# Performance work log

Measured on AMD Instinct MI355X. Metric: run time of the kernel, lower is better.

The kernel has to match this reference:

```python
import jax, jax.numpy as jnp
import numpy as np


def _gelu(v):
    return jax.nn.gelu(v, approximate=False)


def _conv1x1(x, W, b):
    # x: [B, Ci, H, W], W: [Co, Ci]
    return jnp.einsum('bixy,oi->boxy', x, W) + b[None, :, None, None]


def _spectral(x, w1r, w2r, m1, m2):
    # x: [B, Ci, H, W]; w*r: [Ci, Co, m1, m2, 2] (real/imag)
    w1 = w1r[..., 0] + 1j * w1r[..., 1]
    w2 = w2r[..., 0] + 1j * w2r[..., 1]
    B, C, H, W = x.shape
    xf = jnp.fft.rfft2(x)  # [B, Ci, H, W//2+1] complex64
    o1 = jnp.einsum('bixy,ioxy->boxy', xf[:, :, :m1, :m2], w1)
    o2 = jnp.einsum('bixy,ioxy->boxy', xf[:, :, H - m1:, :m2], w2)
    Co = w1.shape[1]
    of = jnp.zeros((B, Co, H, W // 2 + 1), dtype=xf.dtype)
    of = of.at[:, :, :m1, :m2].set(o1)
    of = of.at[:, :, H - m1:, :m2].set(o2)
    return jnp.fft.irfft2(of, s=(H, W))


def _pool(x):
    B, C, H, W = x.shape
    return x.reshape(B, C, H // 2, 2, W // 2, 2).mean(axis=(3, 5))


def _up(x):
    # matches torch F.interpolate(scale_factor=2, mode='bilinear', align_corners=False)
    B, C, H, W = x.shape
    return jax.image.resize(x, (B, C, 2 * H, 2 * W), method='bilinear')


def _forward(x, fcin_w, fcin_b, sc1_w1, sc1_w2, c1_w, c1_b, sc2_w1, sc2_w2, c2_w, c2_b,
             scb_w1, scb_w2, cb_w, cb_b, su2_w1, su2_w2, u2_w, u2_b,
             su1_w1, su1_w2, u1_w, u1_b, fc1_w, fc1_b, fc2_w, fc2_b):
    v = jnp.einsum('bhwi,oi->bhwo', x, fcin_w) + fcin_b   # lift 6 -> width
    v = v.transpose(0, 3, 1, 2)                            # [B, C, H, W]
    x1 = _gelu(_spectral(v, sc1_w1, sc1_w2, 12, 12) + _conv1x1(v, c1_w, c1_b))
    x1d = _pool(x1)
    x2 = _gelu(_spectral(x1d, sc2_w1, sc2_w2, 8, 8) + _conv1x1(x1d, c2_w, c2_b))
    x2d = _pool(x2)
    xb = _gelu(_spectral(x2d, scb_w1, scb_w2, 4, 4) + _conv1x1(x2d, cb_w, cb_b))
    x2c = jnp.concatenate([_up(xb), x2], axis=1)           # [B, 3.5w, H/2, W/2]
    x2o = _gelu(_spectral(x2c, su2_w1, su2_w2, 8, 8) + _conv1x1(x2c, u2_w, u2_b))
    x1c = jnp.concatenate([_up(x2o), x1], axis=1)          # [B, 2.5w, H, W]
    x1o = _gelu(_spectral(x1c, su1_w1, su1_w2, 12, 12) + _conv1x1(x1c, u1_w, u1_b))
    h = x1o.transpose(0, 2, 3, 1)
    h = _gelu(jnp.einsum('bhwi,oi->bhwo', h, fc1_w) + fc1_b)
    return jnp.einsum('bhwi,oi->bhwo', h, fc2_w) + fc2_b   # [B, H, W, 3]


def setup_inputs() -> dict:
    key = jax.random.key(0)
    ks = jax.random.split(key, 20)

    def cw(k, ci, co, m):  # complex spectral weight stored as [...,2] real
        return (1.0 / (ci * co)) * jax.random.normal(k, (ci, co, m, m, 2), dtype=jnp.float32)

    def lin(k, o, i):
        k1, k2 = jax.random.split(k)
        lim = 1.0 / np.sqrt(i)
        return (jax.random.uniform(k1, (o, i), jnp.float32, -lim, lim),
                jax.random.uniform(k2, (o,), jnp.float32, -lim, lim))

    d = {}
    d['x'] = jax.random.normal(ks[0], (4, 256, 256, 6), dtype=jnp.float32)
    d['fcin_w'], d['fcin_b'] = lin(ks[1], 64, 6)
    d['sc1_w1'] = cw(ks[2], 64, 64, 12); d['sc1_w2'] = cw(ks[3], 64, 64, 12)
    d['c1_w'], d['c1_b'] = lin(ks[4], 64, 64)
    d['sc2_w1'] = cw(ks[5], 64, 96, 8); d['sc2_w2'] = cw(ks[6], 64, 96, 8)
    d['c2_w'], d['c2_b'] = lin(ks[7], 96, 64)
    d['scb_w1'] = cw(ks[8], 96, 128, 4); d['scb_w2'] = cw(ks[9], 96, 128, 4)
    d['cb_w'], d['cb_b'] = lin(ks[10], 128, 96)
    d['su2_w1'] = cw(ks[11], 224, 96, 8); d['su2_w2'] = cw(ks[12], 224, 96, 8)
    d['u2_w'], d['u2_b'] = lin(ks[13], 96, 224)
    d['su1_w1'] = cw(ks[14], 160, 64, 12); d['su1_w2'] = cw(ks[15], 160, 64, 12)
    d['u1_w'], d['u1_b'] = lin(ks[16], 64, 160)
    d['fc1_w'], d['fc1_b'] = lin(ks[17], 256, 64)
    d['fc2_w'], d['fc2_b'] = lin(ks[18], 3, 256)
    return d


def reference(x, fcin_w, fcin_b, sc1_w1, sc1_w2, c1_w, c1_b, sc2_w1, sc2_w2, c2_w, c2_b,
              scb_w1, scb_w2, cb_w, cb_b, su2_w1, su2_w2, u2_w, u2_b,
              su1_w1, su1_w2, u1_w, u1_b, fc1_w, fc1_b, fc2_w, fc2_b):
    return _forward(x, fcin_w, fcin_b, sc1_w1, sc1_w2, c1_w, c1_b, sc2_w1, sc2_w2, c2_w, c2_b,
                    scb_w1, scb_w2, cb_w, cb_b, su2_w1, su2_w2, u2_w, u2_b,
                    su1_w1, su1_w2, u1_w, u1_b, fc1_w, fc1_b, fc2_w, fc2_b)
```

## Files before the change

### kernel.cpp

```cpp
#include <hip/hip_runtime.h>
#include <math.h>
#include <cstdio>


__device__ __forceinline__ float gelu_f(float v) {
    return 0.5f * v * (1.0f + erff(v * 0.70710678118654752f));
}

__global__ __launch_bounds__(256) void init_tw_kernel(float2* tw) {
    int t = threadIdx.x;
    tw[t] = make_float2(cospif(t * (1.0f / 128.0f)), sinpif(t * (1.0f / 128.0f)));
}

__global__ __launch_bounds__(256) void transpose_mat_kernel(const float* __restrict__ src,
                                                            float* __restrict__ dst,
                                                            int Co, int Ci) {
    int idx = blockIdx.x * blockDim.x + threadIdx.x;
    if (idx >= Ci * Co) return;
    int o = idx % Co; int i = idx / Co;
    dst[idx] = src[(size_t)o * Ci + i];
}

template <int M2, int SRC, int W_T>
__global__ __launch_bounds__(256, 4) void dftx_kernel(
    const float* __restrict__ U, int C, int Coff, int Ctot,
    int H, int Hs, int Ws,
    const float* __restrict__ liftW, const float* __restrict__ liftB,
    int stepW, const float2* __restrict__ tw, float2* __restrict__ Fx) {
    constexpr int W = W_T;
    constexpr int WS2 = W_T / 2;
    __shared__ float2 twxk[(SRC == 2) ? (WS2 * M2) : (W * M2)];
    int tid = threadIdx.x;
    if constexpr (SRC == 2) {
        for (int t = tid; t < WS2 * M2; t += 256) {
            int j = t / M2, k = t - (t / M2) * M2;
            float wr = 0.f, wi = 0.f;
            auto addE = [&](int xx, float w) {
                float2 e = tw[(xx * k * stepW) & 255];
                wr += w * e.x; wi += w * e.y;
            };
            if (j == 0)            { addE(0, 1.0f); addE(1, 0.75f); addE(2, 0.25f); }
            else if (j == WS2 - 1) { addE(2 * j - 1, 0.25f); addE(2 * j, 0.75f); addE(2 * j + 1, 1.0f); }
            else                   { addE(2 * j - 1, 0.25f); addE(2 * j, 0.75f);
                                     addE(2 * j + 1, 0.75f); addE(2 * j + 2, 0.25f); }
            twxk[t] = make_float2(wr, wi);
        }
    } else {
        for (int t = tid; t < W * M2; t += 256) {
            int x = t / M2, k = t - (t / M2) * M2;
            twxk[t] = tw[(x * k * stepW) & 255];
        }
    }
    __syncthreads();
    int by = blockIdx.x * 4 + (tid >> 6);
    int c = blockIdx.y * 64 + (tid & 63);
    if (c >= C) return;

    const float* rowD = nullptr;
    const float* Sa = nullptr; const float* Sb = nullptr;
    float wy = 0.f, bc = 0.f;
    float w6[6] = {0, 0, 0, 0, 0, 0};
    if constexpr (SRC == 0) {
        rowD = U + (size_t)by * W * C + c;
    } else if constexpr (SRC == 1) {
        bc = liftB[c];
#pragma unroll
        for (int j = 0; j < 6; j++) w6[j] = liftW[c * 6 + j];
    } else {
        int b = by / H, y = by % H;
        float fy = 0.5f * y - 0.25f;
        int y0 = (int)floorf(fy); wy = fy - y0;
        int ya = y0 < 0 ? 0 : y0;
        int yb = (y0 + 1 > Hs - 1) ? Hs - 1 : y0 + 1;
        Sa = U + ((size_t)(b * Hs + ya) * Ws) * C + c;
        Sb = U + ((size_t)(b * Hs + yb) * Ws) * C + c;
    }

    float ar[M2], ai[M2];
#pragma unroll
    for (int k = 0; k < M2; k++) { ar[k] = 0.f; ai[k] = 0.f; }
    if constexpr (SRC == 2) {
        for (int js = 0; js < WS2; js++) {
            float sa = Sa[(size_t)js * C], sb = Sb[(size_t)js * C];
            float u = sa * (1.f - wy) + sb * wy;
            const float4* gp = (const float4*)&twxk[js * M2];
#pragma unroll
            for (int k2 = 0; k2 < M2 / 2; k2++) {
                float4 g4 = gp[k2];
                ar[2 * k2] += u * g4.x;     ai[2 * k2] -= u * g4.y;
                ar[2 * k2 + 1] += u * g4.z; ai[2 * k2 + 1] -= u * g4.w;
            }
        }
    } else {
        for (int x = 0; x < W; x++) {
            float u;
            if constexpr (SRC == 0) {
                u = rowD[(size_t)x * C];
            } else {
                const float* xp = U + ((size_t)by * W + x) * 6;
                u = bc;
#pragma unroll
                for (int j = 0; j < 6; j++) u += w6[j] * xp[j];
            }
            const float4* wp = (const float4*)&twxk[x * M2];
#pragma unroll
            for (int k2 = 0; k2 < M2 / 2; k2++) {
                float4 t4 = wp[k2];
                ar[2 * k2] += u * t4.x;     ai[2 * k2] -= u * t4.y;
                ar[2 * k2 + 1] += u * t4.z; ai[2 * k2 + 1] -= u * t4.w;
            }
        }
    }
    float2* o = Fx + ((size_t)by * M2) * Ctot + Coff + c;
#pragma unroll
    for (int k = 0; k < M2; k++) o[(size_t)k * Ctot] = make_float2(ar[k], ai[k]);
}

template <int M1>
__global__ __launch_bounds__(256, 2) void dfty2_kernel(
    const float2* __restrict__ Fx, int H, int m2, int Ct,
    int stepH, const float2* __restrict__ tw, float2* __restrict__ XF) {
    constexpr int NKY = 2 * M1;
    __shared__ float twc[256], tws[256];
    __shared__ float2 red[3][NKY][64];
    int tid = threadIdx.x;
    for (int t = tid; t < 256; t += 256) {
        float2 v = tw[t]; twc[t] = v.x; tws[t] = v.y;
    }
    __syncthreads();
    int kx = blockIdx.x % m2; int ct = blockIdx.x / m2;
    int b = blockIdx.y;
    int lane = tid & 63, grp = tid >> 6;
    int c = ct * 64 + lane;
    float ar[NKY], ai[NKY];
#pragma unroll
    for (int k = 0; k < NKY; k++) { ar[k] = 0.f; ai[k] = 0.f; }
    if (c < Ct) {
        int ylen = H >> 2;
        int y0 = grp * ylen;
        const float2* base = Fx + ((size_t)(b * H + y0) * m2 + kx) * Ct + c;
        size_t stride = (size_t)m2 * Ct;
        for (int yy = 0; yy < ylen; yy++) {
            float2 f = base[(size_t)yy * stride];
            int a = ((y0 + yy) * stepH) & 255;
            int t = 0;
#pragma unroll
            for (int j = 0; j < M1; j++) {
                float cc = twc[t], ss = tws[t];
                ar[j] += f.x * cc + f.y * ss;
                ai[j] += f.y * cc - f.x * ss;
                t = (t + a) & 255;
            }
            t = (M1 * 256 - M1 * a) & 255;
#pragma unroll
            for (int j = 0; j < M1; j++) {
                float cc = twc[t], ss = tws[t];
                ar[M1 + j] += f.x * cc + f.y * ss;
                ai[M1 + j] += f.y * cc - f.x * ss;
                t = (t + a) & 255;
            }
        }
    }
    if (grp > 0) {
#pragma unroll
        for (int k = 0; k < NKY; k++) red[grp - 1][k][lane] = make_float2(ar[k], ai[k]);
    }
    __syncthreads();
    if (grp == 0 && c < Ct) {
#pragma unroll
        for (int k = 0; k < NKY; k++) {
            float2 r0 = red[0][k][lane], r1 = red[1][k][lane], r2 = red[2][k][lane];
            XF[((size_t)(b * NKY + k) * m2 + kx) * Ct + c] =
                make_float2(ar[k] + r0.x + r1.x + r2.x, ai[k] + r0.y + r1.y + r2.y);
        }
    }
}

__global__ __launch_bounds__(128, 2) void modemix2_kernel(
    const float2* __restrict__ XF,
    const float* __restrict__ w1f, const float* __restrict__ w2f,
    int Ci, int Co, int m1, int m2, float2* __restrict__ OF) {
    __shared__ float2 xsm[4][224];
    int mode = blockIdx.x;
    int nmode = 2 * m1 * m2;
    for (int t = threadIdx.x; t < 4 * Ci; t += blockDim.x) {
        int b = t / Ci, i = t - b * Ci;
        xsm[b][i] = XF[((size_t)b * nmode + mode) * Ci + i];
    }
    __syncthreads();
    int o = threadIdx.x;
    if (o >= Co) return;
    int kx = mode % m2; int kyi = mode / m2;
    const float2* w = (const float2*)((kyi < m1) ? w1f : w2f);
    int ky = (kyi < m1) ? kyi : (kyi - m1);
    float ar0 = 0, ai0 = 0, ar1 = 0, ai1 = 0, ar2 = 0, ai2 = 0, ar3 = 0, ai3 = 0;
    for (int i = 0; i < Ci; i++) {
        float2 wv = w[(((size_t)i * Co + o) * m1 + ky) * m2 + kx];
        float2 a = xsm[0][i], b2 = xsm[1][i], c2 = xsm[2][i], d2 = xsm[3][i];
        ar0 += a.x * wv.x - a.y * wv.y;  ai0 += a.x * wv.y + a.y * wv.x;
        ar1 += b2.x * wv.x - b2.y * wv.y; ai1 += b2.x * wv.y + b2.y * wv.x;
        ar2 += c2.x * wv.x - c2.y * wv.y; ai2 += c2.x * wv.y + c2.y * wv.x;
        ar3 += d2.x * wv.x - d2.y * wv.y; ai3 += d2.x * wv.y + d2.y * wv.x;
    }
    OF[((size_t)0 * nmode + mode) * Co + o] = make_float2(ar0, ai0);
    OF[((size_t)1 * nmode + mode) * Co + o] = make_float2(ar1, ai1);
    OF[((size_t)2 * nmode + mode) * Co + o] = make_float2(ar2, ai2);
    OF[((size_t)3 * nmode + mode) * Co + o] = make_float2(ar3, ai3);
}

__global__ __launch_bounds__(256, 4) void idfty_kernel(
    const float2* __restrict__ OF, int H, int m1, int m2, int Co,
    int stepH, const float2* __restrict__ tw, float2* __restrict__ Gy, int N) {
    __shared__ float twc[256], tws[256];
    for (int t = threadIdx.x; t < 256; t += blockDim.x) {
        float2 v = tw[t]; twc[t] = v.x; tws[t] = v.y;
    }
    __syncthreads();
    int idx = blockIdx.x * blockDim.x + threadIdx.x;
    if (idx >= N) return;
    int o = idx % Co; int r = idx / Co;
    int kx = r % m2;  r /= m2;
    int y = r % H;    int b = r / H;
    float accr = 0.f, acci = 0.f;
    for (int kyi = 0; kyi < 2 * m1; kyi++) {
        int ky = (kyi < m1) ? kyi : (H - 2 * m1 + kyi);
        int t = (ky * y * stepH) & 255;
        float2 f = OF[((size_t)(b * 2 * m1 + kyi) * m2 + kx) * Co + o];
        float cc = twc[t], ss = tws[t];
        accr += f.x * cc - f.y * ss;
        acci += f.x * ss + f.y * cc;
    }
    Gy[idx] = make_float2(accr, acci);
}

template <int SRCA, bool HASB, int CO, int CI, int M2, int PG, int MINW>
__global__ __launch_bounds__((CO / 8) * PG, MINW) void synth_kernel(
    const float2* __restrict__ Gy,
    const float* __restrict__ A, int CA, int HsA, int WsA,
    const float* __restrict__ UB, int CB,
    const float* __restrict__ liftW, const float* __restrict__ liftB,
    const float* __restrict__ WcT, const float* __restrict__ bias,
    int H, int W, int stepW, float invHW,
    const float2* __restrict__ tw, float* __restrict__ out) {
    constexpr int OO = CO / 8;
    constexpr int BLK = OO * PG;
    constexpr int P = PG * 4;
    constexpr int CIP = CI + 1;
    __shared__ float xs[P][CIP];
    __shared__ float2 twL[M2][P];
    int tid = threadIdx.x;
    int pix0 = blockIdx.x * P;
    int x0 = pix0 % W;  int by = pix0 / W;
    for (int t = tid; t < M2 * P; t += BLK) {
        int k = t / P, p = t - (t / P) * P;
        float2 v = tw[((x0 + p) * k * stepW) & 255];
        float s = ((k == 0) ? 1.f : 2.f) * invHW;
        twL[k][p] = make_float2(s * v.x, s * v.y);
    }
    for (int t = tid; t < P * CI; t += BLK) {
        int p = t / CI, i = t - p * CI;
        int pix = pix0 + p;
        float val;
        if (HASB && i >= CA) {
            val = UB[(size_t)pix * CB + (i - CA)];
        } else if constexpr (SRCA == 0) {
            val = A[(size_t)pix * CA + i];
        } else if constexpr (SRCA == 1) {
            const float* xp = A + (size_t)pix * 6;
            float a = liftB[i];
#pragma unroll
            for (int j = 0; j < 6; j++) a += xp[j] * liftW[i * 6 + j];
            val = a;
        } else {
            int xx = pix % W; int r = pix / W; int y = r % H; int b = r / H;
            float fy = 0.5f * y - 0.25f, fx = 0.5f * xx - 0.25f;
            int y0 = (int)floorf(fy); float wy = fy - y0;
            int x0i = (int)floorf(fx); float wx = fx - x0i;
            int ya = y0 < 0 ? 0 : y0;
            int yb = (y0 + 1 > HsA - 1) ? HsA - 1 : y0 + 1;
            int xa = x0i < 0 ? 0 : x0i;
            int xb2 = (x0i + 1 > WsA - 1) ? WsA - 1 : x0i + 1;
            const float* base = A + ((size_t)b * HsA * WsA) * CA + i;
            float v00 = base[((size_t)ya * WsA + xa) * CA];
            float v01 = base[((size_t)ya * WsA + xb2) * CA];
            float v10 = base[((size_t)yb * WsA + xa) * CA];
            float v11 = base[((size_t)yb * WsA + xb2) * CA];
            val = (1.f - wy) * ((1.f - wx) * v00 + wx * v01) +
                  wy * ((1.f - wx) * v10 + wx * v11);
        }
        xs[p][i] = val;
    }
    __syncthreads();
    int oo = tid % OO, pg = tid / OO;
    float acc[4][8];
#pragma unroll
    for (int q = 0; q < 4; q++)
#pragma unroll
        for (int j = 0; j < 8; j++) acc[q][j] = 0.f;
    const float2* grow = Gy + ((size_t)by * M2) * CO + oo * 8;
#pragma unroll
    for (int k = 0; k < M2; k++) {
        float4 g0 = *(const float4*)&grow[(size_t)k * CO + 0];
        float4 g1 = *(const float4*)&grow[(size_t)k * CO + 2];
        float4 g2 = *(const float4*)&grow[(size_t)k * CO + 4];
        float4 g3 = *(const float4*)&grow[(size_t)k * CO + 6];
#pragma unroll
        for (int q = 0; q < 4; q++) {
            float2 tq = twL[k][pg * 4 + q];
            acc[q][0] += g0.x * tq.x - g0.y * tq.y;
            acc[q][1] += g0.z * tq.x - g0.w * tq.y;
            acc[q][2] += g1.x * tq.x - g1.y * tq.y;
            acc[q][3] += g1.z * tq.x - g1.w * tq.y;
            acc[q][4] += g2.x * tq.x - g2.y * tq.y;
            acc[q][5] += g2.z * tq.x - g2.w * tq.y;
            acc[q][6] += g3.x * tq.x - g3.y * tq.y;
            acc[q][7] += g3.z * tq.x - g3.w * tq.y;
        }
    }
    const float* wrow = WcT + oo * 8;
#pragma unroll 4
    for (int i = 0; i < CI; i++) {
        float4 wa = *(const float4*)&wrow[(size_t)i * CO];
        float4 wb = *(const float4*)&wrow[(size_t)i * CO + 4];
#pragma unroll
        for (int q = 0; q < 4; q++) {
            float a = xs[pg * 4 + q][i];
            acc[q][0] += a * wa.x; acc[q][1] += a * wa.y;
            acc[q][2] += a * wa.z; acc[q][3] += a * wa.w;
            acc[q][4] += a * wb.x; acc[q][5] += a * wb.y;
            acc[q][6] += a * wb.z; acc[q][7] += a * wb.w;
        }
    }
    float4 ba = *(const float4*)&bias[oo * 8];
    float4 bb = *(const float4*)&bias[oo * 8 + 4];
#pragma unroll
    for (int q = 0; q < 4; q++) {
        int pix = pix0 + pg * 4 + q;
        float4 r0, r1;
        r0.x = gelu_f(acc[q][0] + ba.x);
        r0.y = gelu_f(acc[q][1] + ba.y);
        r0.z = gelu_f(acc[q][2] + ba.z);
        r0.w = gelu_f(acc[q][3] + ba.w);
        r1.x = gelu_f(acc[q][4] + bb.x);
        r1.y = gelu_f(acc[q][5] + bb.y);
        r1.z = gelu_f(acc[q][6] + bb.z);
        r1.w = gelu_f(acc[q][7] + bb.w);
        *(float4*)&out[(size_t)pix * CO + oo * 8] = r0;
        *(float4*)&out[(size_t)pix * CO + oo * 8 + 4] = r1;
    }
}

__global__ __launch_bounds__(256, 2) void head_kernel(
    const float* __restrict__ xin, const float* __restrict__ fc1t,
    const float* __restrict__ fc1b, const float* __restrict__ fc2w,
    const float* __restrict__ fc2b, float* __restrict__ out) {
    __shared__ float xs[16][65];
    __shared__ float red[64][49];
    int tid = threadIdx.x;
    int pix0 = blockIdx.x * 16;
    const float* src = xin + (size_t)pix0 * 64;
    for (int t = tid; t < 16 * 64; t += 256) xs[t >> 6][t & 63] = src[t];
    __syncthreads();
    int jq = tid & 63, pg = tid >> 6;
    float acc[4][4];
#pragma unroll
    for (int q = 0; q < 4; q++)
#pragma unroll
        for (int j = 0; j < 4; j++) acc[q][j] = 0.f;
    const float* wrow = fc1t + jq * 4;
    for (int i = 0; i < 64; i++) {
        float4 w = *(const float4*)&wrow[(size_t)i * 256];
#pragma unroll
        for (int q = 0; q < 4; q++) {
            float a = xs[pg * 4 + q][i];
            acc[q][0] += a * w.x; acc[q][1] += a * w.y;
            acc[q][2] += a * w.z; acc[q][3] += a * w.w;
        }
    }
    float4 b1 = *(const float4*)&fc1b[jq * 4];
    float4 w20 = *(const float4*)&fc2w[0 * 256 + jq * 4];
    float4 w21 = *(const float4*)&fc2w[1 * 256 + jq * 4];
    float4 w22 = *(const float4*)&fc2w[2 * 256 + jq * 4];
#pragma unroll
    for (int q = 0; q < 4; q++) {
        float h0 = gelu_f(acc[q][0] + b1.x);
        float h1 = gelu_f(acc[q][1] + b1.y);
        float h2 = gelu_f(acc[q][2] + b1.z);
        float h3 = gelu_f(acc[q][3] + b1.w);
        int col = (pg * 4 + q) * 3;
        red[jq][col + 0] = h0 * w20.x + h1 * w20.y + h2 * w20.z + h3 * w20.w;
        red[jq][col + 1] = h0 * w21.x + h1 * w21.y + h2 * w21.z + h3 * w21.w;
        red[jq][col + 2] = h0 * w22.x + h1 * w22.y + h2 * w22.z + h3 * w22.w;
    }
    __syncthreads();
    if (tid < 48) {
        float s = 0.f;
        for (int j = 0; j < 64; j++) s += red[j][tid];
        int px = tid / 3, o3 = tid - 3 * px;
        out[(size_t)(pix0 + px) * 3 + o3] = s + fc2b[o3];
    }
}

__global__ __launch_bounds__(256, 4) void pool_kernel(
    const float* __restrict__ in, float* __restrict__ out,
    int H2, int W2, int C, int N) {
    int idx = blockIdx.x * blockDim.x + threadIdx.x;
    if (idx >= N) return;
    int c = idx % C; int r = idx / C;
    int xo = r % W2; r /= W2;
    int yo = r % H2; int b = r / H2;
    int W = W2 * 2;
    const float* p = in + (((size_t)(b * (H2 * 2) + 2 * yo) * W) + 2 * xo) * C + c;
    float v = p[0] + p[C] + p[(size_t)W * C] + p[(size_t)W * C + C];
    out[idx] = 0.25f * v;
}


static inline unsigned nb_(size_t n, int b) { return (unsigned)((n + b - 1) / b); }

extern "C" void kernel_launch(void* const* d_in, const int* in_sizes, int n_in,
                              void* d_out, int out_size, void* d_ws, size_t ws_size,
                              hipStream_t stream) {
    (void)in_sizes; (void)n_in; (void)out_size;
    const float* x      = (const float*)d_in[0];
    const float* fcin_w = (const float*)d_in[1];
    const float* fcin_b = (const float*)d_in[2];
    const float* sc1_w1 = (const float*)d_in[3];
    const float* sc1_w2 = (const float*)d_in[4];
    const float* c1_w   = (const float*)d_in[5];
    const float* c1_b   = (const float*)d_in[6];
    const float* sc2_w1 = (const float*)d_in[7];
    const float* sc2_w2 = (const float*)d_in[8];
    const float* c2_w   = (const float*)d_in[9];
    const float* c2_b   = (const float*)d_in[10];
    const float* scb_w1 = (const float*)d_in[11];
    const float* scb_w2 = (const float*)d_in[12];
    const float* cb_w   = (const float*)d_in[13];
    const float* cb_b   = (const float*)d_in[14];
    const float* su2_w1 = (const float*)d_in[15];
    const float* su2_w2 = (const float*)d_in[16];
    const float* u2_w   = (const float*)d_in[17];
    const float* u2_b   = (const float*)d_in[18];
    const float* su1_w1 = (const float*)d_in[19];
    const float* su1_w2 = (const float*)d_in[20];
    const float* u1_w   = (const float*)d_in[21];
    const float* u1_b   = (const float*)d_in[22];
    const float* fc1_w  = (const float*)d_in[23];
    const float* fc1_b  = (const float*)d_in[24];
    const float* fc2_w  = (const float*)d_in[25];
    const float* fc2_b  = (const float*)d_in[26];
    float* out = (float*)d_out;

    float* wsf = (float*)d_ws;
    size_t off = 0;
    auto alloc = [&](size_t nfloats) -> float* {
        float* p = wsf + off;
        off += (nfloats + 63) & ~(size_t)63;
        return p;
    };

    float2* tw = (float2*)alloc(512);
    float* c1t  = alloc(64 * 64);
    float* c2t  = alloc(64 * 96);
    float* cbt  = alloc(96 * 128);
    float* u2t  = alloc(224 * 96);
    float* u1t  = alloc(160 * 64);
    float* fc1t = alloc(64 * 256);

    float* x1  = alloc((size_t)4 * 256 * 256 * 64);
    float* x1d = alloc((size_t)4 * 128 * 128 * 64);
    float* x2  = alloc((size_t)4 * 128 * 128 * 96);
    float* xb  = alloc((size_t)4 * 64 * 64 * 128);
    float* x2o = alloc((size_t)4 * 128 * 128 * 96);

    float2* Fx = (float2*)alloc((size_t)2 * 4 * 256 * 12 * 160);
    float2* XF = (float2*)alloc((size_t)2 * 4 * 24 * 12 * 160);
    float2* OF = (float2*)alloc((size_t)2 * 4 * 24 * 12 * 128);
    float2* Gy = (float2*)alloc((size_t)2 * 4 * 256 * 12 * 96);

    size_t need = off * sizeof(float);
    if (ws_size < need) {
        fprintf(stderr, "[FNO2d] workspace too small: need %zu bytes, have %zu\n",
                need, ws_size);
        return;
    }
    float* x2d = x1d;

    init_tw_kernel<<<1, 256, 0, stream>>>(tw);
    transpose_mat_kernel<<<nb_(64 * 64, 256), 256, 0, stream>>>(c1_w, c1t, 64, 64);
    transpose_mat_kernel<<<nb_(64 * 96, 256), 256, 0, stream>>>(c2_w, c2t, 96, 64);
    transpose_mat_kernel<<<nb_(96 * 128, 256), 256, 0, stream>>>(cb_w, cbt, 128, 96);
    transpose_mat_kernel<<<nb_(224 * 96, 256), 256, 0, stream>>>(u2_w, u2t, 96, 224);
    transpose_mat_kernel<<<nb_(160 * 64, 256), 256, 0, stream>>>(u1_w, u1t, 64, 160);
    transpose_mat_kernel<<<nb_(64 * 256, 256), 256, 0, stream>>>(fc1_w, fc1t, 256, 64);

    int N;

    dftx_kernel<12, 1, 256><<<dim3(256, 1), 256, 0, stream>>>(
        x, 64, 0, 64, 256, 0, 0, fcin_w, fcin_b, 1, tw, Fx);
    dfty2_kernel<12><<<dim3(12, 4), 256, 0, stream>>>(Fx, 256, 12, 64, 1, tw, XF);
    modemix2_kernel<<<288, 128, 0, stream>>>(XF, sc1_w1, sc1_w2, 64, 64, 12, 12, OF);
    N = 4 * 256 * 12 * 64;
    idfty_kernel<<<nb_(N, 256), 256, 0, stream>>>(OF, 256, 12, 12, 64, 1, tw, Gy, N);
    synth_kernel<1, false, 64, 64, 12, 16, 3><<<4 * 256 * 256 / 64, 128, 0, stream>>>(
        Gy, x, 64, 0, 0, nullptr, 0, fcin_w, fcin_b, c1t, c1_b,
        256, 256, 1, 1.0f / 65536.0f, tw, x1);
    N = 4 * 128 * 128 * 64;
    pool_kernel<<<nb_(N, 256), 256, 0, stream>>>(x1, x1d, 128, 128, 64, N);

    dftx_kernel<8, 0, 128><<<dim3(128, 1), 256, 0, stream>>>(
        x1d, 64, 0, 64, 128, 0, 0, nullptr, nullptr, 2, tw, Fx);
    dfty2_kernel<8><<<dim3(8, 4), 256, 0, stream>>>(Fx, 128, 8, 64, 2, tw, XF);
    modemix2_kernel<<<128, 128, 0, stream>>>(XF, sc2_w1, sc2_w2, 64, 96, 8, 8, OF);
    N = 4 * 128 * 8 * 96;
    idfty_kernel<<<nb_(N, 256), 256, 0, stream>>>(OF, 128, 8, 8, 96, 2, tw, Gy, N);
    synth_kernel<0, false, 96, 64, 8, 16, 2><<<4 * 128 * 128 / 64, 192, 0, stream>>>(
        Gy, x1d, 64, 0, 0, nullptr, 0, nullptr, nullptr, c2t, c2_b,
        128, 128, 2, 1.0f / 16384.0f, tw, x2);
    N = 4 * 64 * 64 * 96;
    pool_kernel<<<nb_(N, 256), 256, 0, stream>>>(x2, x2d, 64, 64, 96, N);

    dftx_kernel<4, 0, 64><<<dim3(64, 2), 256, 0, stream>>>(
        x2d, 96, 0, 96, 64, 0, 0, nullptr, nullptr, 4, tw, Fx);
    dfty2_kernel<4><<<dim3(4 * 2, 4), 256, 0, stream>>>(Fx, 64, 4, 96, 4, tw, XF);
    modemix2_kernel<<<32, 128, 0, stream>>>(XF, scb_w1, scb_w2, 96, 128, 4, 4, OF);
    N = 4 * 64 * 4 * 128;
    idfty_kernel<<<nb_(N, 256), 256, 0, stream>>>(OF, 64, 4, 4, 128, 4, tw, Gy, N);
    synth_kernel<0, false, 128, 96, 4, 8, 2><<<4 * 64 * 64 / 32, 128, 0, stream>>>(
        Gy, x2d, 96, 0, 0, nullptr, 0, nullptr, nullptr, cbt, cb_b,
        64, 64, 4, 1.0f / 4096.0f, tw, xb);

    dftx_kernel<8, 2, 128><<<dim3(128, 2), 256, 0, stream>>>(
        xb, 128, 0, 224, 128, 64, 64, nullptr, nullptr, 2, tw, Fx);
    dftx_kernel<8, 0, 128><<<dim3(128, 2), 256, 0, stream>>>(
        x2, 96, 128, 224, 128, 0, 0, nullptr, nullptr, 2, tw, Fx);
    dfty2_kernel<8><<<dim3(8 * 4, 4), 256, 0, stream>>>(Fx, 128, 8, 224, 2, tw, XF);
    modemix2_kernel<<<128, 128, 0, stream>>>(XF, su2_w1, su2_w2, 224, 96, 8, 8, OF);
    N = 4 * 128 * 8 * 96;
    idfty_kernel<<<nb_(N, 256), 256, 0, stream>>>(OF, 128, 8, 8, 96, 2, tw, Gy, N);
    synth_kernel<2, true, 96, 224, 8, 16, 2><<<4 * 128 * 128 / 64, 192, 0, stream>>>(
        Gy, xb, 128, 64, 64, x2, 96, nullptr, nullptr, u2t, u2_b,
        128, 128, 2, 1.0f / 16384.0f, tw, x2o);

    dftx_kernel<12, 2, 256><<<dim3(256, 2), 256, 0, stream>>>(
        x2o, 96, 0, 160, 256, 128, 128, nullptr, nullptr, 1, tw, Fx);
    dftx_kernel<12, 0, 256><<<dim3(256, 1), 256, 0, stream>>>(
        x1, 64, 96, 160, 256, 0, 0, nullptr, nullptr, 1, tw, Fx);
    dfty2_kernel<12><<<dim3(12 * 3, 4), 256, 0, stream>>>(Fx, 256, 12, 160, 1, tw, XF);
    modemix2_kernel<<<288, 128, 0, stream>>>(XF, su1_w1, su1_w2, 160, 64, 12, 12, OF);
    N = 4 * 256 * 12 * 64;
    idfty_kernel<<<nb_(N, 256), 256, 0, stream>>>(OF, 256, 12, 12, 64, 1, tw, Gy, N);
    synth_kernel<2, true, 64, 160, 12, 16, 2><<<4 * 256 * 256 / 64, 128, 0, stream>>>(
        Gy, x2o, 96, 128, 128, x1, 64, nullptr, nullptr, u1t, u1_b,
        256, 256, 1, 1.0f / 65536.0f, tw, x1);

    head_kernel<<<4 * 256 * 256 / 16, 256, 0, stream>>>(
        x1, fc1t, fc1_b, fc2_w, fc2_b, out);
}
```

Baseline: 2.017 ms.

## Retile synth kernel to 4 outputs per thread with split-channel LDS staging

The synth kernel now gives each thread 4 output channels instead of 8 and uses 32 pixels per block, which halves the accumulator registers and doubles the block count. Input channels are staged into shared memory in two halves separated by extra barriers, halving the LDS footprint. The goal is higher occupancy and more parallelism. The cost is twice the reads of the inverse-DFT Gy rows and weights per output, plus extra synchronisation.

```diff
diff --git a/kernel.cpp b/kernel.cpp
--- a/kernel.cpp
+++ b/kernel.cpp
@@ -233,8 +233,8 @@
     Gy[idx] = make_float2(accr, acci);
 }
 
-template <int SRCA, bool HASB, int CO, int CI, int M2, int PG, int MINW>
-__global__ __launch_bounds__((CO / 8) * PG, MINW) void synth_kernel(
+template <int SRCA, bool HASB, int CO, int CI, int M2, int MINW>
+__global__ __launch_bounds__((CO / 4) * 8, MINW) void synth_kernel(
     const float2* __restrict__ Gy,
     const float* __restrict__ A, int CA, int HsA, int WsA,
     const float* __restrict__ UB, int CB,
@@ -242,35 +242,29 @@
     const float* __restrict__ WcT, const float* __restrict__ bias,
     int H, int W, int stepW, float invHW,
     const float2* __restrict__ tw, float* __restrict__ out) {
-    constexpr int OO = CO / 8;
-    constexpr int BLK = OO * PG;
-    constexpr int P = PG * 4;
-    constexpr int CIP = CI + 1;
+    constexpr int OQ = CO / 4;
+    constexpr int BLK = OQ * 8;
+    constexpr int P = 32;
+    constexpr int CIH = CI / 2;
+    constexpr int CIP = CIH + 1;
     __shared__ float xs[P][CIP];
     __shared__ float2 twL[M2][P];
     int tid = threadIdx.x;
     int pix0 = blockIdx.x * P;
     int x0 = pix0 % W;  int by = pix0 / W;
-    for (int t = tid; t < M2 * P; t += BLK) {
-        int k = t / P, p = t - (t / P) * P;
-        float2 v = tw[((x0 + p) * k * stepW) & 255];
-        float s = ((k == 0) ? 1.f : 2.f) * invHW;
-        twL[k][p] = make_float2(s * v.x, s * v.y);
-    }
-    for (int t = tid; t < P * CI; t += BLK) {
-        int p = t / CI, i = t - p * CI;
+
+    auto srcval = [&](int p, int i) -> float {
         int pix = pix0 + p;
-        float val;
         if (HASB && i >= CA) {
-            val = UB[(size_t)pix * CB + (i - CA)];
+            return UB[(size_t)pix * CB + (i - CA)];
         } else if constexpr (SRCA == 0) {
-            val = A[(size_t)pix * CA + i];
+            return A[(size_t)pix * CA + i];
         } else if constexpr (SRCA == 1) {
             const float* xp = A + (size_t)pix * 6;
             float a = liftB[i];
 #pragma unroll
             for (int j = 0; j < 6; j++) a += xp[j] * liftW[i * 6 + j];
-            val = a;
+            return a;
         } else {
             int xx = pix % W; int r = pix / W; int y = r % H; int b = r / H;
             float fy = 0.5f * y - 0.25f, fx = 0.5f * xx - 0.25f;
@@ -285,68 +279,85 @@
             float v01 = base[((size_t)ya * WsA + xb2) * CA];
             float v10 = base[((size_t)yb * WsA + xa) * CA];
             float v11 = base[((size_t)yb * WsA + xb2) * CA];
-            val = (1.f - wy) * ((1.f - wx) * v00 + wx * v01) +
-                  wy * ((1.f - wx) * v10 + wx * v11);
-        }
-        xs[p][i] = val;
-    }
-    __syncthreads();
-    int oo = tid % OO, pg = tid / OO;
-    float acc[4][8];
+            return (1.f - wy) * ((1.f - wx) * v00 + wx * v01) +
+                   wy * ((1.f - wx) * v10 + wx * v11);
+        }
+    };
+
+    for (int t = tid; t < M2 * P; t += BLK) {
+        int k = t / P, p = t - (t / P) * P;
+        float2 v = tw[((x0 + p) * k * stepW) & 255];
+        float s = ((k == 0) ? 1.f : 2.f) * invHW;
+        twL[k][p] = make_float2(s * v.x, s * v.y);
+    }
+    for (int t = tid; t < P * CIH; t += BLK) {
+        int p = t / CIH, il = t - (t / CIH) * CIH;
+        xs[p][il] = srcval(p, il);
+    }
+    __syncthreads();
+
+    int oq = tid % OQ, pg = tid / OQ;
+    float acc[4][4];
 #pragma unroll
     for (int q = 0; q < 4; q++)
 #pragma unroll
-        for (int j = 0; j < 8; j++) acc[q][j] = 0.f;
-    const float2* grow = Gy + ((size_t)by * M2) * CO + oo * 8;
+        for (int j = 0; j < 4; j++) acc[q][j] = 0.f;
+    const float2* grow = Gy + ((size_t)by * M2) * CO + oq * 4;
 #pragma unroll
     for (int k = 0; k < M2; k++) {
-        float4 g0 = *(const float4*)&grow[(size_t)k * CO + 0];
-        float4 g1 = *(const float4*)&grow[(size_t)k * CO + 2];
-        float4 g2 = *(const float4*)&grow[(size_t)k * CO + 4];
-        float4 g3 = *(const float4*)&grow[(size_t)k * CO + 6];
+        float4 ga = *(const float4*)&grow[(size_t)k * CO];
+        float4 gb = *(const float4*)&grow[(size_t)k * CO + 2];
 #pragma unroll
         for (int q = 0; q < 4; q++) {
             float2 tq = twL[k][pg * 4 + q];
-            acc[q][0] += g0.x * tq.x - g0.y * tq.y;
-            acc[q][1] += g0.z * tq.x - g0.w * tq.y;
-            acc[q][2] += g1.x * tq.x - g1.y * tq.y;
-            acc[q][3] += g1.z * tq.x - g1.w * tq.y;
-            acc[q][4] += g2.x * tq.x - g2.y * tq.y;
-            acc[q][5] += g2.z * tq.x - g2.w * tq.y;
-            acc[q][6] += g3.x * tq.x - g3.y * tq.y;
-            acc[q][7] += g3.z * tq.x - g3.w * tq.y;
-        }
-    }
-    const float* wrow = WcT + oo * 8;
-#pragma unroll 4
-    for (int i = 0; i < CI; i++) {
-        float4 wa = *(const float4*)&wrow[(size_t)i * CO];
-        float4 wb = *(const float4*)&wrow[(size_t)i * CO + 4];
-#pragma unroll
-        for (int q = 0; q < 4; q++) {
-            float a = xs[pg * 4 + q][i];
-            acc[q][0] += a * wa.x; acc[q][1] += a * wa.y;
-            acc[q][2] += a * wa.z; acc[q][3] += a * wa.w;
-            acc[q][4] += a * wb.x; acc[q][5] += a * wb.y;
-            acc[q][6] += a * wb.z; acc[q][7] += a * wb.w;
-        }
-    }
-    float4 ba = *(const float4*)&bias[oo * 8];
-    float4 bb = *(const float4*)&bias[oo * 8 + 4];
+            acc[q][0] += ga.x * tq.x - ga.y * tq.y;
+            acc[q][1] += ga.z * tq.x - ga.w * tq.y;
+            acc[q][2] += gb.x * tq.x - gb.y * tq.y;
+            acc[q][3] += gb.z * tq.x - gb.w * tq.y;
+        }
+    }
+    {
+        const float* wrow = WcT + oq * 4;
+#pragma unroll 8
+        for (int il = 0; il < CIH; il++) {
+            float4 w = *(const float4*)&wrow[(size_t)il * CO];
+#pragma unroll
+            for (int q = 0; q < 4; q++) {
+                float a = xs[pg * 4 + q][il];
+                acc[q][0] += a * w.x; acc[q][1] += a * w.y;
+                acc[q][2] += a * w.z; acc[q][3] += a * w.w;
+            }
+        }
+    }
+    __syncthreads();
+    for (int t = tid; t < P * CIH; t += BLK) {
+        int p = t / CIH, il = t - (t / CIH) * CIH;
+        xs[p][il] = srcval(p, CIH + il);
+    }
+    __syncthreads();
+    {
+        const float* wrow = WcT + (size_t)CIH * CO + oq * 4;
+#pragma unroll 8
+        for (int il = 0; il < CIH; il++) {
+            float4 w = *(const float4*)&wrow[(size_t)il * CO];
+#pragma unroll
+            for (int q = 0; q < 4; q++) {
+                float a = xs[pg * 4 + q][il];
+                acc[q][0] += a * w.x; acc[q][1] += a * w.y;
+                acc[q][2] += a * w.z; acc[q][3] += a * w.w;
+            }
+        }
+    }
+    float4 bb = *(const float4*)&bias[oq * 4];
 #pragma unroll
     for (int q = 0; q < 4; q++) {
         int pix = pix0 + pg * 4 + q;
-        float4 r0, r1;
-        r0.x = gelu_f(acc[q][0] + ba.x);
-        r0.y = gelu_f(acc[q][1] + ba.y);
-        r0.z = gelu_f(acc[q][2] + ba.z);
-        r0.w = gelu_f(acc[q][3] + ba.w);
-        r1.x = gelu_f(acc[q][4] + bb.x);
-        r1.y = gelu_f(acc[q][5] + bb.y);
-        r1.z = gelu_f(acc[q][6] + bb.z);
-        r1.w = gelu_f(acc[q][7] + bb.w);
-        *(float4*)&out[(size_t)pix * CO + oo * 8] = r0;
-        *(float4*)&out[(size_t)pix * CO + oo * 8 + 4] = r1;
+        float4 r;
+        r.x = gelu_f(acc[q][0] + bb.x);
+        r.y = gelu_f(acc[q][1] + bb.y);
+        r.z = gelu_f(acc[q][2] + bb.z);
+        r.w = gelu_f(acc[q][3] + bb.w);
+        *(float4*)&out[(size_t)pix * CO + oq * 4] = r;
     }
 }
 
@@ -502,7 +513,7 @@
     modemix2_kernel<<<288, 128, 0, stream>>>(XF, sc1_w1, sc1_w2, 64, 64, 12, 12, OF);
     N = 4 * 256 * 12 * 64;
     idfty_kernel<<<nb_(N, 256), 256, 0, stream>>>(OF, 256, 12, 12, 64, 1, tw, Gy, N);
-    synth_kernel<1, false, 64, 64, 12, 16, 3><<<4 * 256 * 256 / 64, 128, 0, stream>>>(
+    synth_kernel<1, false, 64, 64, 12, 4><<<4 * 256 * 256 / 32, 128, 0, stream>>>(
         Gy, x, 64, 0, 0, nullptr, 0, fcin_w, fcin_b, c1t, c1_b,
         256, 256, 1, 1.0f / 65536.0f, tw, x1);
     N = 4 * 128 * 128 * 64;
@@ -514,7 +525,7 @@
     modemix2_kernel<<<128, 128, 0, stream>>>(XF, sc2_w1, sc2_w2, 64, 96, 8, 8, OF);
     N = 4 * 128 * 8 * 96;
     idfty_kernel<<<nb_(N, 256), 256, 0, stream>>>(OF, 128, 8, 8, 96, 2, tw, Gy, N);
-    synth_kernel<0, false, 96, 64, 8, 16, 2><<<4 * 128 * 128 / 64, 192, 0, stream>>>(
+    synth_kernel<0, false, 96, 64, 8, 4><<<4 * 128 * 128 / 32, 192, 0, stream>>>(
         Gy, x1d, 64, 0, 0, nullptr, 0, nullptr, nullptr, c2t, c2_b,
         128, 128, 2, 1.0f / 16384.0f, tw, x2);
     N = 4 * 64 * 64 * 96;
@@ -526,7 +537,7 @@
     modemix2_kernel<<<32, 128, 0, stream>>>(XF, scb_w1, scb_w2, 96, 128, 4, 4, OF);
     N = 4 * 64 * 4 * 128;
     idfty_kernel<<<nb_(N, 256), 256, 0, stream>>>(OF, 64, 4, 4, 128, 4, tw, Gy, N);
-    synth_kernel<0, false, 128, 96, 4, 8, 2><<<4 * 64 * 64 / 32, 128, 0, stream>>>(
+    synth_kernel<0, false, 128, 96, 4, 4><<<4 * 64 * 64 / 32, 256, 0, stream>>>(
         Gy, x2d, 96, 0, 0, nullptr, 0, nullptr, nullptr, cbt, cb_b,
         64, 64, 4, 1.0f / 4096.0f, tw, xb);
 
@@ -538,7 +549,7 @@
     modemix2_kernel<<<128, 128, 0, stream>>>(XF, su2_w1, su2_w2, 224, 96, 8, 8, OF);
     N = 4 * 128 * 8 * 96;
     idfty_kernel<<<nb_(N, 256), 256, 0, stream>>>(OF, 128, 8, 8, 96, 2, tw, Gy, N);
-    synth_kernel<2, true, 96, 224, 8, 16, 2><<<4 * 128 * 128 / 64, 192, 0, stream>>>(
+    synth_kernel<2, true, 96, 224, 8, 4><<<4 * 128 * 128 / 32, 192, 0, stream>>>(
         Gy, xb, 128, 64, 64, x2, 96, nullptr, nullptr, u2t, u2_b,
         128, 128, 2, 1.0f / 16384.0f, tw, x2o);
 
@@ -550,7 +561,7 @@
     modemix2_kernel<<<288, 128, 0, stream>>>(XF, su1_w1, su1_w2, 160, 64, 12, 12, OF);
     N = 4 * 256 * 12 * 64;
     idfty_kernel<<<nb_(N, 256), 256, 0, stream>>>(OF, 256, 12, 12, 64, 1, tw, Gy, N);
-    synth_kernel<2, true, 64, 160, 12, 16, 2><<<4 * 256 * 256 / 64, 128, 0, stream>>>(
+    synth_kernel<2, true, 64, 160, 12, 4><<<4 * 256 * 256 / 32, 128, 0, stream>>>(
         Gy, x2o, 96, 128, 128, x1, 64, nullptr, nullptr, u1t, u1_b,
         256, 256, 1, 1.0f / 65536.0f, tw, x1);
 
```

Result: faster. 1.857 ms (-8.0%).
